# Kernel optimization log

Hardware: AMD Instinct MI355X
Metric: run time of the kernel (lower is better)

The kernel has to match this reference:

```python
import jax, jax.numpy as jnp
import numpy as np

NUM_HEADS = 16
KEY_SIZE = 64
HEAD_SIZE = 64


def setup_inputs() -> dict:
    key = jax.random.key(0)
    ks = jax.random.split(key, 8)
    B, S, D = 2, 2048, 1024
    s = 1.0 / np.sqrt(D)
    return {
        "q": jax.random.normal(ks[0], (B, S, D), jnp.float32),
        "k": jax.random.normal(ks[1], (B, S, D), jnp.float32),
        "v": jax.random.normal(ks[2], (B, S, D), jnp.float32),
        "v_mask": jax.random.randint(ks[3], (B, S), 0, 2, jnp.int32),
        "Wq": jax.random.normal(ks[4], (D, NUM_HEADS * KEY_SIZE), jnp.float32) * s,
        "Wk": jax.random.normal(ks[5], (D, NUM_HEADS * KEY_SIZE), jnp.float32) * s,
        "Wv": jax.random.normal(ks[6], (D, NUM_HEADS * HEAD_SIZE), jnp.float32) * s,
    }


def reference(q, k, v, v_mask, Wq, Wk, Wv):
    B, Sq, _ = q.shape
    Sk = k.shape[1]
    # projections + split heads: [B, S, H, d]
    qw = (q @ Wq).reshape(B, Sq, NUM_HEADS, KEY_SIZE)
    kw = (k @ Wk).reshape(B, Sk, NUM_HEADS, KEY_SIZE)
    vw = (v @ Wv).reshape(B, Sk, NUM_HEADS, HEAD_SIZE)
    # scores [B, H, Sq, Sk]
    a = jnp.einsum('bqhd,bkhd->bhqk', qw, kw) / np.sqrt(KEY_SIZE).astype(np.float32)
    # additive mask over key axis: x*m - (1-m)*1e12
    m = v_mask.astype(a.dtype)[:, None, None, :]
    a = a * m - (1.0 - m) * 1e12
    a = jax.nn.softmax(a, axis=-1)
    # output [B, Sq, H*head_size]
    o = jnp.einsum('bhqk,bkhd->bqhd', a, vw)
    return o.reshape(B, Sq, NUM_HEADS * HEAD_SIZE)
```

## Files before the change

### kernel.cpp

```cpp
#include <hip/hip_runtime.h>
#include <hip/hip_bf16.h>


#define SEQ 2048
#define DIM 1024
#define NPROJ 1024

typedef __bf16 bf16x8 __attribute__((ext_vector_type(8)));
typedef float floatx4 __attribute__((ext_vector_type(4)));
typedef float floatx16 __attribute__((ext_vector_type(16)));

__device__ inline unsigned short f2bf_bits(float x) {
  __hip_bfloat16 h = __float2bfloat16(x);
  return __builtin_bit_cast(unsigned short, h);
}

__device__ __forceinline__ void gload_lds16(const void* g, void* l) {
  __builtin_amdgcn_global_load_lds((const __attribute__((address_space(1))) void*)g,
                                   (__attribute__((address_space(3))) void*)l, 16, 0, 0);
}

__global__ __launch_bounds__(256) void cvt_x(
    const float* __restrict__ q, const float* __restrict__ k, const float* __restrict__ v,
    unsigned short* __restrict__ xb)
{
  const float* X = blockIdx.z == 0 ? q : (blockIdx.z == 1 ? k : v);
  unsigned short* O = xb + (size_t)blockIdx.z * 4096 * 1024;
  int i0 = blockIdx.x * 256 + threadIdx.x;
  #pragma unroll
  for (int it = 0; it < 4; ++it) {
    int i = i0 + it * 262144;
    float4 f = *reinterpret_cast<const float4*>(&X[(size_t)i * 4]);
    ushort4 o;
    o.x = f2bf_bits(f.x); o.y = f2bf_bits(f.y);
    o.z = f2bf_bits(f.z); o.w = f2bf_bits(f.w);
    *reinterpret_cast<ushort4*>(&O[(size_t)i * 4]) = o;
  }
}

__global__ __launch_bounds__(256) void transpose_w(
    const float* __restrict__ Wq, const float* __restrict__ Wk, const float* __restrict__ Wv,
    unsigned short* __restrict__ WqT, unsigned short* __restrict__ WkT, unsigned short* __restrict__ WvT)
{
  const float* W = blockIdx.z == 0 ? Wq : (blockIdx.z == 1 ? Wk : Wv);
  unsigned short* WT = blockIdx.z == 0 ? WqT : (blockIdx.z == 1 ? WkT : WvT);
  const float sc = (blockIdx.z == 0) ? 0.1803368801f : 1.0f;
  __shared__ float tile[64][65];
  const int k0 = blockIdx.x * 64;
  const int n0 = blockIdx.y * 64;
  const int t = threadIdx.x;
  #pragma unroll
  for (int it = 0; it < 4; ++it) {
    int idx = t + (it << 8);
    int r = idx >> 4, c4 = (idx & 15) << 2;
    float4 v = *reinterpret_cast<const float4*>(&W[(k0 + r) * DIM + n0 + c4]);
    tile[r][c4 + 0] = v.x; tile[r][c4 + 1] = v.y;
    tile[r][c4 + 2] = v.z; tile[r][c4 + 3] = v.w;
  }
  __syncthreads();
  #pragma unroll
  for (int it = 0; it < 4; ++it) {
    int idx = t + (it << 8);
    int r = idx >> 4, c4 = (idx & 15) << 2;
    ushort4 o;
    o.x = f2bf_bits(tile[c4 + 0][r] * sc);
    o.y = f2bf_bits(tile[c4 + 1][r] * sc);
    o.z = f2bf_bits(tile[c4 + 2][r] * sc);
    o.w = f2bf_bits(tile[c4 + 3][r] * sc);
    *reinterpret_cast<ushort4*>(&WT[(n0 + r) * DIM + k0 + c4]) = o;
  }
}

__global__ __launch_bounds__(256, 4) void proj_gemm(
    const unsigned short* __restrict__ xb,
    const unsigned short* __restrict__ WqT, const unsigned short* __restrict__ WkT,
    const unsigned short* __restrict__ WvT,
    unsigned short* __restrict__ qw, unsigned short* __restrict__ kw, unsigned short* __restrict__ vw)
{
  const unsigned short* X = xb + (size_t)blockIdx.z * 4096 * 1024;
  const unsigned short* WT = blockIdx.z == 0 ? WqT : (blockIdx.z == 1 ? WkT : WvT);
  unsigned short* Y = blockIdx.z == 0 ? qw : (blockIdx.z == 1 ? kw : vw);

  __shared__ unsigned short Al[2][128 * 32];
  __shared__ unsigned short Bl[2][128 * 32];

  const int m0 = blockIdx.x * 128, n0 = blockIdx.y * 128;
  const int t = threadIdx.x;
  const int lane = t & 63;
  const int wid = t >> 6;
  const int wm = (wid >> 1) << 6, wn = (wid & 1) << 6;
  const int qd = lane >> 4, ln = lane & 15;

  auto stage = [&](int ks, int bi) {
    const int kb = ks << 6;
    #pragma unroll
    for (int i = 0; i < 2; ++i) {
      int p = t + (i << 8);
      int r = p >> 2, c = p & 3;
      int f = (r + (r >> 2)) & 3;
      gload_lds16((const char*)X + (size_t)(m0 + r) * 2048 + kb + ((c ^ f) << 4),
                  (char*)&Al[bi][0] + p * 16);
      gload_lds16((const char*)WT + (size_t)(n0 + r) * 2048 + kb + ((c ^ f) << 4),
                  (char*)&Bl[bi][0] + p * 16);
    }
  };

  floatx4 acc[4][4] = {};
  stage(0, 0);

  for (int ks = 0; ks < 32; ++ks) {
    __syncthreads();
    if (ks + 1 < 32) stage(ks + 1, (ks + 1) & 1);
    const int bi = ks & 1;
    bf16x8 af[4], bfr[4];
    #pragma unroll
    for (int mb = 0; mb < 4; ++mb) {
      int m = wm + mb * 16 + ln;
      int fm = (m + (m >> 2)) & 3;
      af[mb] = *reinterpret_cast<const bf16x8*>(&Al[bi][m * 32 + ((qd ^ fm) << 3)]);
    }
    #pragma unroll
    for (int nb = 0; nb < 4; ++nb) {
      int n = wn + nb * 16 + ln;
      int fn = (n + (n >> 2)) & 3;
      bfr[nb] = *reinterpret_cast<const bf16x8*>(&Bl[bi][n * 32 + ((qd ^ fn) << 3)]);
    }
    #pragma unroll
    for (int mb = 0; mb < 4; ++mb)
      #pragma unroll
      for (int nb = 0; nb < 4; ++nb)
        acc[mb][nb] = __builtin_amdgcn_mfma_f32_16x16x32_bf16(af[mb], bfr[nb], acc[mb][nb], 0, 0, 0);
  }
  #pragma unroll
  for (int mb = 0; mb < 4; ++mb)
    #pragma unroll
    for (int nb = 0; nb < 4; ++nb)
      #pragma unroll
      for (int i = 0; i < 4; ++i) {
        int m = m0 + wm + mb * 16 + qd * 4 + i;
        int n = n0 + wn + nb * 16 + ln;
        Y[(size_t)m * NPROJ + n] = f2bf_bits(acc[mb][nb][i]);
      }
}

__global__ __launch_bounds__(256) void transpose_v(
    const unsigned short* __restrict__ vw, const int* __restrict__ vmask,
    unsigned short* __restrict__ vt, unsigned short* __restrict__ mb)
{
  if (blockIdx.y == 0 && blockIdx.x < 16) {
    int i = blockIdx.x * 256 + threadIdx.x;
    mb[i] = vmask[i] ? 0x3F80 : 0;
  }
  __shared__ unsigned short tile[64 * 64];
  const int t = threadIdx.x;
  const int s0 = blockIdx.x * 64;
  const int bh = blockIdx.y;
  const int b = bh >> 4, h = bh & 15;
  #pragma unroll
  for (int it = 0; it < 2; ++it) {
    int p = t + (it << 8);
    int s = p >> 3, c = p & 7;
    int cp = (c + (s >> 3) + (s & 7)) & 7;
    int4 d = *reinterpret_cast<const int4*>(&vw[(size_t)(b * SEQ + s0 + s) * NPROJ + h * 64 + c * 8]);
    if (vmask[b * SEQ + s0 + s] == 0) { d.x = 0; d.y = 0; d.z = 0; d.w = 0; }
    *reinterpret_cast<int4*>(&tile[s * 64 + cp * 8]) = d;
  }
  __syncthreads();
  #pragma unroll
  for (int it = 0; it < 2; ++it) {
    int d = (t >> 3) + (it << 5), sc = t & 7;
    struct { alignas(16) unsigned short u[8]; } o;
    #pragma unroll
    for (int j = 0; j < 8; ++j) {
      int s = sc * 8 + j;
      int cp = ((d >> 3) + (s >> 3) + (s & 7)) & 7;
      o.u[j] = tile[s * 64 + cp * 8 + (d & 7)];
    }
    *reinterpret_cast<int4*>(&vt[(size_t)(bh * 64 + d) * SEQ + s0 + sc * 8]) =
        *reinterpret_cast<const int4*>(o.u);
  }
}

__global__ __launch_bounds__(512, 4) void attn_fwd(
    const unsigned short* __restrict__ qw, const unsigned short* __restrict__ kw,
    const unsigned short* __restrict__ vt, const unsigned short* __restrict__ mb,
    float* __restrict__ out)
{
  extern __shared__ char smem[];
  unsigned short* Kl = (unsigned short*)smem;
  unsigned short* Vl = (unsigned short*)(smem + 16384);
  unsigned short* Ml = (unsigned short*)(smem + 32768);

  const int t = threadIdx.x, lane = t & 63, wid = t >> 6;
  const int l5 = lane & 31, hi = lane >> 5;
  const int qh = wid >> 1, kh = wid & 1;
  const int bh = blockIdx.x;
  const int q0 = blockIdx.y * 128;
  const int b = bh >> 4, h = bh & 15;
  const int base = b * SEQ;

  auto stage = [&](int kt, int bi) {
    const int k0 = kt << 6;
    int rb = wid * 8;
    int r = rb + (lane >> 3);
    int rsrc = (r & ~12) | ((r & 4) << 1) | ((r & 8) >> 1);
    int sw = ((lane & 7) ^ (r & 7)) << 4;
    gload_lds16((const char*)kw + ((size_t)((base + k0 + rsrc) * NPROJ + h * 64) << 1) + sw,
                (char*)&Kl[bi * 4096] + rb * 128);
    gload_lds16((const char*)vt + ((size_t)((bh * 64 + r) * SEQ + k0) << 1) + sw,
                (char*)&Vl[bi * 4096] + rb * 128);
    if (wid == 7 && lane < 8)
      gload_lds16((const char*)mb + ((size_t)(base + k0 + lane * 8) << 1), (char*)&Ml[bi * 64]);
  };

  bf16x8 qf[4];
  {
    const unsigned short* qptr =
        qw + (size_t)(base + q0 + qh * 32 + l5) * NPROJ + h * 64 + hi * 8;
    #pragma unroll
    for (int kk = 0; kk < 4; ++kk)
      qf[kk] = *reinterpret_cast<const bf16x8*>(qptr + kk * 16);
  }

  floatx16 oa0 = {}, oa1 = {}, la = {};
  stage(0, 0);

  #pragma unroll 2
  for (int kt = 0; kt < SEQ / 64; ++kt) {
    __syncthreads();
    if (kt + 1 < SEQ / 64) stage(kt + 1, (kt + 1) & 1);
    const int bi = kt & 1;

    floatx16 s = {};
    __builtin_amdgcn_s_setprio(1);
    #pragma unroll
    for (int kk = 0; kk < 4; ++kk) {
      int ph = ((kk * 2 + hi) ^ (l5 & 7)) << 3;
      bf16x8 kf = *reinterpret_cast<const bf16x8*>(&Kl[bi * 4096 + (kh * 32 + l5) * 64 + ph]);
      s = __builtin_amdgcn_mfma_f32_32x32x16_bf16(kf, qf[kk], s, 0, 0, 0);
    }
    __builtin_amdgcn_s_setprio(0);

    float pe[16];
    #pragma unroll
    for (int r = 0; r < 16; ++r) pe[r] = __builtin_amdgcn_exp2f(s[r]);

    #pragma unroll
    for (int kk = 0; kk < 2; ++kk) {
      struct alignas(16) { unsigned short u[8]; } pk;
      #pragma unroll
      for (int j = 0; j < 8; ++j) pk.u[j] = f2bf_bits(pe[8 * kk + j]);
      bf16x8 pa = __builtin_bit_cast(bf16x8, pk);
      int ch = ((4 * kh + 2 * kk + hi) ^ (l5 & 7)) << 3;
      bf16x8 v0 = *reinterpret_cast<const bf16x8*>(&Vl[bi * 4096 + l5 * 64 + ch]);
      bf16x8 v1 = *reinterpret_cast<const bf16x8*>(&Vl[bi * 4096 + (32 + l5) * 64 + ch]);
      bf16x8 mf = *reinterpret_cast<const bf16x8*>(&Ml[bi * 64 + kh * 32 + kk * 16 + hi * 8]);
      __builtin_amdgcn_s_setprio(1);
      oa0 = __builtin_amdgcn_mfma_f32_32x32x16_bf16(pa, v0, oa0, 0, 0, 0);
      oa1 = __builtin_amdgcn_mfma_f32_32x32x16_bf16(pa, v1, oa1, 0, 0, 0);
      la  = __builtin_amdgcn_mfma_f32_32x32x16_bf16(pa, mf, la, 0, 0, 0);
      __builtin_amdgcn_s_setprio(0);
    }
  }

  __syncthreads();
  float* Mg = (float*)smem;
  if (kh == 1) {
    #pragma unroll
    for (int r = 0; r < 16; ++r) {
      int row = qh * 32 + (r & 3) + ((r >> 2) << 3) + (hi << 2);
      Mg[row * 66 + l5] = oa0[r];
      Mg[row * 66 + 32 + l5] = oa1[r];
      if (l5 == 0) Mg[row * 66 + 64] = la[r];
    }
  }
  __syncthreads();
  if (kh == 0) {
    #pragma unroll
    for (int r = 0; r < 16; ++r) {
      int row = qh * 32 + (r & 3) + ((r >> 2) << 3) + (hi << 2);
      float o0 = oa0[r] + Mg[row * 66 + l5];
      float o1 = oa1[r] + Mg[row * 66 + 32 + l5];
      float inv = 1.0f / (la[r] + Mg[row * 66 + 64]);
      size_t o = (size_t)(base + q0 + row) * NPROJ + h * 64;
      out[o + l5] = o0 * inv;
      out[o + 32 + l5] = o1 * inv;
    }
  }
}

extern "C" void kernel_launch(void* const* d_in, const int* in_sizes, int n_in,
                              void* d_out, int out_size, void* d_ws, size_t ws_size,
                              hipStream_t stream) {
  const float* q  = (const float*)d_in[0];
  const float* k  = (const float*)d_in[1];
  const float* v  = (const float*)d_in[2];
  const int* vm   = (const int*)d_in[3];
  const float* Wq = (const float*)d_in[4];
  const float* Wk = (const float*)d_in[5];
  const float* Wv = (const float*)d_in[6];
  float* out = (float*)d_out;

  unsigned short* ws = (unsigned short*)d_ws;
  unsigned short* WqT = ws + ((size_t)0 << 20);
  unsigned short* WkT = ws + ((size_t)1 << 20);
  unsigned short* WvT = ws + ((size_t)2 << 20);
  unsigned short* qw  = ws + ((size_t)3 << 20);
  unsigned short* kw  = ws + ((size_t)7 << 20);
  unsigned short* vw  = ws + ((size_t)11 << 20);
  unsigned short* xb  = ws + ((size_t)15 << 20);
  unsigned short* vt  = ws + ((size_t)15 << 20);
  unsigned short* mbv = WqT;

  cvt_x<<<dim3(1024, 1, 3), 256, 0, stream>>>(q, k, v, xb);
  transpose_w<<<dim3(16, 16, 3), 256, 0, stream>>>(Wq, Wk, Wv, WqT, WkT, WvT);
  proj_gemm<<<dim3(32, 8, 3), 256, 0, stream>>>(xb, WqT, WkT, WvT, qw, kw, vw);
  transpose_v<<<dim3(32, 32), 256, 0, stream>>>(vw, vm, vt, mbv);
  attn_fwd<<<dim3(32, 16), 512, 33792, stream>>>(qw, kw, vt, mbv, out);
}
```

Before: 102.9 us.

## Give each attention wave two query sub-tiles to reuse K/V LDS fragments

The attention kernel now runs 256 threads per block instead of 512. Each wave computes two 32-row query sub-tiles, so every K, V and mask fragment read from LDS feeds two MFMAs. The staging loop issues two loads per wave to cover the tile, and the epilogue reduces both sub-tiles. This cuts LDS read traffic per MFMA and halves block-wide barrier participants, at the cost of doubled accumulator registers and fewer waves available to hide latency.

Result: no change. 102.9 us (-0.0%).

```diff
diff --git a/kernel.cpp b/kernel.cpp
--- a/kernel.cpp
+++ b/kernel.cpp
@@ -181,7 +181,7 @@
   }
 }
 
-__global__ __launch_bounds__(512, 4) void attn_fwd(
+__global__ __launch_bounds__(256, 2) void attn_fwd(
     const unsigned short* __restrict__ qw, const unsigned short* __restrict__ kw,
     const unsigned short* __restrict__ vt, const unsigned short* __restrict__ mb,
     float* __restrict__ out)
@@ -201,28 +201,35 @@
 
   auto stage = [&](int kt, int bi) {
     const int k0 = kt << 6;
-    int rb = wid * 8;
-    int r = rb + (lane >> 3);
-    int rsrc = (r & ~12) | ((r & 4) << 1) | ((r & 8) >> 1);
-    int sw = ((lane & 7) ^ (r & 7)) << 4;
-    gload_lds16((const char*)kw + ((size_t)((base + k0 + rsrc) * NPROJ + h * 64) << 1) + sw,
-                (char*)&Kl[bi * 4096] + rb * 128);
-    gload_lds16((const char*)vt + ((size_t)((bh * 64 + r) * SEQ + k0) << 1) + sw,
-                (char*)&Vl[bi * 4096] + rb * 128);
-    if (wid == 7 && lane < 8)
+    #pragma unroll
+    for (int i = 0; i < 2; ++i) {
+      int rb = wid * 16 + i * 8;
+      int r = rb + (lane >> 3);
+      int rsrc = (r & ~12) | ((r & 4) << 1) | ((r & 8) >> 1);
+      int sw = ((lane & 7) ^ (r & 7)) << 4;
+      gload_lds16((const char*)kw + ((size_t)((base + k0 + rsrc) * NPROJ + h * 64) << 1) + sw,
+                  (char*)&Kl[bi * 4096] + rb * 128);
+      gload_lds16((const char*)vt + ((size_t)((bh * 64 + r) * SEQ + k0) << 1) + sw,
+                  (char*)&Vl[bi * 4096] + rb * 128);
+    }
+    if (wid == 3 && lane < 8)
       gload_lds16((const char*)mb + ((size_t)(base + k0 + lane * 8) << 1), (char*)&Ml[bi * 64]);
   };
 
-  bf16x8 qf[4];
+  bf16x8 qfa[4], qfb[4];
   {
-    const unsigned short* qptr =
-        qw + (size_t)(base + q0 + qh * 32 + l5) * NPROJ + h * 64 + hi * 8;
-    #pragma unroll
-    for (int kk = 0; kk < 4; ++kk)
-      qf[kk] = *reinterpret_cast<const bf16x8*>(qptr + kk * 16);
-  }
-
-  floatx16 oa0 = {}, oa1 = {}, la = {};
+    const unsigned short* qpa =
+        qw + (size_t)(base + q0 + qh * 64 + l5) * NPROJ + h * 64 + hi * 8;
+    const unsigned short* qpb = qpa + (size_t)32 * NPROJ;
+    #pragma unroll
+    for (int kk = 0; kk < 4; ++kk) {
+      qfa[kk] = *reinterpret_cast<const bf16x8*>(qpa + kk * 16);
+      qfb[kk] = *reinterpret_cast<const bf16x8*>(qpb + kk * 16);
+    }
+  }
+
+  floatx16 oa0a = {}, oa1a = {}, laa = {};
+  floatx16 oa0b = {}, oa1b = {}, lab = {};
   stage(0, 0);
 
   #pragma unroll 2
@@ -231,34 +238,45 @@
     if (kt + 1 < SEQ / 64) stage(kt + 1, (kt + 1) & 1);
     const int bi = kt & 1;
 
-    floatx16 s = {};
+    floatx16 sa = {}, sb = {};
     __builtin_amdgcn_s_setprio(1);
     #pragma unroll
     for (int kk = 0; kk < 4; ++kk) {
       int ph = ((kk * 2 + hi) ^ (l5 & 7)) << 3;
       bf16x8 kf = *reinterpret_cast<const bf16x8*>(&Kl[bi * 4096 + (kh * 32 + l5) * 64 + ph]);
-      s = __builtin_amdgcn_mfma_f32_32x32x16_bf16(kf, qf[kk], s, 0, 0, 0);
+      sa = __builtin_amdgcn_mfma_f32_32x32x16_bf16(kf, qfa[kk], sa, 0, 0, 0);
+      sb = __builtin_amdgcn_mfma_f32_32x32x16_bf16(kf, qfb[kk], sb, 0, 0, 0);
     }
     __builtin_amdgcn_s_setprio(0);
 
-    float pe[16];
-    #pragma unroll
-    for (int r = 0; r < 16; ++r) pe[r] = __builtin_amdgcn_exp2f(s[r]);
+    float pea[16], peb[16];
+    #pragma unroll
+    for (int r = 0; r < 16; ++r) {
+      pea[r] = __builtin_amdgcn_exp2f(sa[r]);
+      peb[r] = __builtin_amdgcn_exp2f(sb[r]);
+    }
 
     #pragma unroll
     for (int kk = 0; kk < 2; ++kk) {
-      struct alignas(16) { unsigned short u[8]; } pk;
+      struct alignas(16) { unsigned short u[8]; } pka, pkb;
       #pragma unroll
-      for (int j = 0; j < 8; ++j) pk.u[j] = f2bf_bits(pe[8 * kk + j]);
-      bf16x8 pa = __builtin_bit_cast(bf16x8, pk);
+      for (int j = 0; j < 8; ++j) {
+        pka.u[j] = f2bf_bits(pea[8 * kk + j]);
+        pkb.u[j] = f2bf_bits(peb[8 * kk + j]);
+      }
+      bf16x8 paa = __builtin_bit_cast(bf16x8, pka);
+      bf16x8 pab = __builtin_bit_cast(bf16x8, pkb);
       int ch = ((4 * kh + 2 * kk + hi) ^ (l5 & 7)) << 3;
       bf16x8 v0 = *reinterpret_cast<const bf16x8*>(&Vl[bi * 4096 + l5 * 64 + ch]);
       bf16x8 v1 = *reinterpret_cast<const bf16x8*>(&Vl[bi * 4096 + (32 + l5) * 64 + ch]);
       bf16x8 mf = *reinterpret_cast<const bf16x8*>(&Ml[bi * 64 + kh * 32 + kk * 16 + hi * 8]);
       __builtin_amdgcn_s_setprio(1);
-      oa0 = __builtin_amdgcn_mfma_f32_32x32x16_bf16(pa, v0, oa0, 0, 0, 0);
-      oa1 = __builtin_amdgcn_mfma_f32_32x32x16_bf16(pa, v1, oa1, 0, 0, 0);
-      la  = __builtin_amdgcn_mfma_f32_32x32x16_bf16(pa, mf, la, 0, 0, 0);
+      oa0a = __builtin_amdgcn_mfma_f32_32x32x16_bf16(paa, v0, oa0a, 0, 0, 0);
+      oa1a = __builtin_amdgcn_mfma_f32_32x32x16_bf16(paa, v1, oa1a, 0, 0, 0);
+      laa  = __builtin_amdgcn_mfma_f32_32x32x16_bf16(paa, mf, laa, 0, 0, 0);
+      oa0b = __builtin_amdgcn_mfma_f32_32x32x16_bf16(pab, v0, oa0b, 0, 0, 0);
+      oa1b = __builtin_amdgcn_mfma_f32_32x32x16_bf16(pab, v1, oa1b, 0, 0, 0);
+      lab  = __builtin_amdgcn_mfma_f32_32x32x16_bf16(pab, mf, lab, 0, 0, 0);
       __builtin_amdgcn_s_setprio(0);
     }
   }
@@ -268,23 +286,33 @@
   if (kh == 1) {
     #pragma unroll
     for (int r = 0; r < 16; ++r) {
-      int row = qh * 32 + (r & 3) + ((r >> 2) << 3) + (hi << 2);
-      Mg[row * 66 + l5] = oa0[r];
-      Mg[row * 66 + 32 + l5] = oa1[r];
-      if (l5 == 0) Mg[row * 66 + 64] = la[r];
+      int m = (r & 3) + ((r >> 2) << 3) + (hi << 2);
+      int rowa = qh * 64 + m, rowb = qh * 64 + 32 + m;
+      Mg[rowa * 66 + l5] = oa0a[r];
+      Mg[rowa * 66 + 32 + l5] = oa1a[r];
+      Mg[rowb * 66 + l5] = oa0b[r];
+      Mg[rowb * 66 + 32 + l5] = oa1b[r];
+      if (l5 == 0) { Mg[rowa * 66 + 64] = laa[r]; Mg[rowb * 66 + 64] = lab[r]; }
     }
   }
   __syncthreads();
   if (kh == 0) {
     #pragma unroll
     for (int r = 0; r < 16; ++r) {
-      int row = qh * 32 + (r & 3) + ((r >> 2) << 3) + (hi << 2);
-      float o0 = oa0[r] + Mg[row * 66 + l5];
-      float o1 = oa1[r] + Mg[row * 66 + 32 + l5];
-      float inv = 1.0f / (la[r] + Mg[row * 66 + 64]);
-      size_t o = (size_t)(base + q0 + row) * NPROJ + h * 64;
-      out[o + l5] = o0 * inv;
-      out[o + 32 + l5] = o1 * inv;
+      int m = (r & 3) + ((r >> 2) << 3) + (hi << 2);
+      int rowa = qh * 64 + m, rowb = qh * 64 + 32 + m;
+      float o0a = oa0a[r] + Mg[rowa * 66 + l5];
+      float o1a = oa1a[r] + Mg[rowa * 66 + 32 + l5];
+      float inva = 1.0f / (laa[r] + Mg[rowa * 66 + 64]);
+      size_t oa_ = (size_t)(base + q0 + rowa) * NPROJ + h * 64;
+      out[oa_ + l5] = o0a * inva;
+      out[oa_ + 32 + l5] = o1a * inva;
+      float o0b = oa0b[r] + Mg[rowb * 66 + l5];
+      float o1b = oa1b[r] + Mg[rowb * 66 + 32 + l5];
+      float invb = 1.0f / (lab[r] + Mg[rowb * 66 + 64]);
+      size_t ob_ = (size_t)(base + q0 + rowb) * NPROJ + h * 64;
+      out[ob_ + l5] = o0b * invb;
+      out[ob_ + 32 + l5] = o1b * invb;
     }
   }
 }
@@ -316,5 +344,5 @@
   transpose_w<<<dim3(16, 16, 3), 256, 0, stream>>>(Wq, Wk, Wv, WqT, WkT, WvT);
   proj_gemm<<<dim3(32, 8, 3), 256, 0, stream>>>(xb, WqT, WkT, WvT, qw, kw, vw);
   transpose_v<<<dim3(32, 32), 256, 0, stream>>>(vw, vm, vt, mbv);
-  attn_fwd<<<dim3(32, 16), 512, 33792, stream>>>(qw, kw, vt, mbv, out);
-}
+  attn_fwd<<<dim3(32, 16), 256, 33792, stream>>>(qw, kw, vt, mbv, out);
+}
```
